# Optimization experiments

Hardware: AMD Instinct MI355X
Metric: run time of the kernel (lower is better)

## Reference

```python
import jax, jax.numpy as jnp
import numpy as np

D_MODEL = 1024
NUM_HEADS = 16
D_K = D_MODEL // NUM_HEADS
B, S = 4, 4096


def setup_inputs() -> dict:
    key = jax.random.key(0)
    ks = jax.random.split(key, 12)
    sc = 1.0 / np.sqrt(D_MODEL)
    inp = {
        "query": jax.random.normal(ks[0], (B, S, D_MODEL), dtype=jnp.float32),
        "key": jax.random.normal(ks[1], (B, S, D_MODEL), dtype=jnp.float32),
        "value": jax.random.normal(ks[2], (B, S, D_MODEL), dtype=jnp.float32),
        "w_q": jax.random.normal(ks[3], (D_MODEL, D_MODEL), dtype=jnp.float32) * sc,
        "b_q": jax.random.normal(ks[4], (D_MODEL,), dtype=jnp.float32) * sc,
        "w_k": jax.random.normal(ks[5], (D_MODEL, D_MODEL), dtype=jnp.float32) * sc,
        "b_k": jax.random.normal(ks[6], (D_MODEL,), dtype=jnp.float32) * sc,
        "w_v": jax.random.normal(ks[7], (D_MODEL, D_MODEL), dtype=jnp.float32) * sc,
        "b_v": jax.random.normal(ks[8], (D_MODEL,), dtype=jnp.float32) * sc,
        "w_o": jax.random.normal(ks[9], (D_MODEL, D_MODEL), dtype=jnp.float32) * sc,
        "b_o": jax.random.normal(ks[10], (D_MODEL,), dtype=jnp.float32) * sc,
    }
    return inp


def reference(query, key, value, w_q, b_q, w_k, b_k, w_v, b_v, w_o, b_o):
    b, s, _ = query.shape
    # projections (torch Linear: x @ W.T + b)
    Q = query @ w_q.T + b_q
    K = key @ w_k.T + b_k
    V = value @ w_v.T + b_v
    # elu+1 feature map
    Q = jax.nn.elu(Q) + 1.0
    K = jax.nn.elu(K) + 1.0
    # [b, h, s, d]
    Q = Q.reshape(b, s, NUM_HEADS, D_K).transpose(0, 2, 1, 3)
    K = K.reshape(b, s, NUM_HEADS, D_K).transpose(0, 2, 1, 3)
    V = V.reshape(b, s, NUM_HEADS, D_K).transpose(0, 2, 1, 3)
    # KV outer-sum: [b, h, d, d]
    KV = jnp.einsum("bhsd,bhse->bhde", K, V)
    Z = jnp.einsum("bhsd,bhde->bhse", Q, KV)  # [b, h, s, d]
    Ksum = K.sum(axis=-2)  # [b, h, d]
    D = jnp.einsum("bhsd,bhd->bhs", Q, Ksum)[..., None]  # [b, h, s, 1]
    Z = Z / (D + 1e-6)
    Z = Z.transpose(0, 2, 1, 3).reshape(b, s, D_MODEL)
    return Z @ w_o.T + b_o
```

## Files before the change

### kernel.cpp

```cpp
#include <hip/hip_runtime.h>
#include <stdint.h>

#define DM 1024
#define NH 16
#define DKH 64
#define BB 4
#define SS 4096
#define MM (BB*SS)

typedef __bf16 bf16x8 __attribute__((ext_vector_type(8)));
typedef float f32x4 __attribute__((ext_vector_type(4)));

__device__ __forceinline__ float bf2f(ushort u) {
  union { uint32_t i; float f; } v; v.i = ((uint32_t)u) << 16; return v.f;
}
__device__ __forceinline__ ushort f2bf(float f) {
  union { float f; uint32_t i; } v; v.f = f;
  uint32_t x = v.i;
  uint32_t r = (x + 0x7fffu + ((x >> 16) & 1u)) >> 16;
  return (ushort)r;
}
__device__ __forceinline__ void unpack8(uint4 u, float* o) {
  o[0] = bf2f((ushort)(u.x & 0xffff)); o[1] = bf2f((ushort)(u.x >> 16));
  o[2] = bf2f((ushort)(u.y & 0xffff)); o[3] = bf2f((ushort)(u.y >> 16));
  o[4] = bf2f((ushort)(u.z & 0xffff)); o[5] = bf2f((ushort)(u.z >> 16));
  o[6] = bf2f((ushort)(u.w & 0xffff)); o[7] = bf2f((ushort)(u.w >> 16));
}
__device__ __forceinline__ void unpack4(uint2 u, float* o) {
  o[0] = bf2f((ushort)(u.x & 0xffff)); o[1] = bf2f((ushort)(u.x >> 16));
  o[2] = bf2f((ushort)(u.y & 0xffff)); o[3] = bf2f((ushort)(u.y >> 16));
}

#define GLL16(g, l) __builtin_amdgcn_global_load_lds( \
    (__attribute__((address_space(1))) void*)(g), \
    (__attribute__((address_space(3))) void*)(l), 16, 0, 0)

__global__ void cast_w4(const float* __restrict__ s0, const float* __restrict__ s1,
                        const float* __restrict__ s2, const float* __restrict__ s3,
                        ushort* __restrict__ d0, ushort* __restrict__ d1,
                        ushort* __restrict__ d2, ushort* __restrict__ d3) {
  const int which = blockIdx.x >> 10;
  const int i = ((blockIdx.x & 1023) * 256 + threadIdx.x) * 4;
  const float* src = which == 0 ? s0 : (which == 1 ? s1 : (which == 2 ? s2 : s3));
  ushort* dst = which == 0 ? d0 : (which == 1 ? d1 : (which == 2 ? d2 : d3));
  float4 v = *reinterpret_cast<const float4*>(src + i);
  ushort4 o; o.x = f2bf(v.x); o.y = f2bf(v.y); o.z = f2bf(v.z); o.w = f2bf(v.w);
  *reinterpret_cast<ushort4*>(dst + i) = o;
}

template<int MODE>
__global__ __launch_bounds__(512, 2) void gemm8p(
    const ushort* __restrict__ A, const ushort* __restrict__ Bw,
    const float* __restrict__ bias, void* __restrict__ Cout) {
  constexpr int K = DM, N = DM;
  constexpr int NT = K / 32;
  __shared__ ushort smem[4][2][256 * 32];
  const int t = threadIdx.x;
  const int lane = t & 63;
  const int w = t >> 6;
  const int id = blockIdx.y * gridDim.x + blockIdx.x;
  const int cpx = (gridDim.x * gridDim.y) >> 3;
  const int swz = (id & 7) * cpx + (id >> 3);
  const int bx = swz % gridDim.x;
  const int by = swz / gridDim.x;
  const int m0 = by * 256, n0 = bx * 256;
  const int wm = w >> 2, wn = w & 3;
  const int fr = lane & 15;
  const int slot = lane >> 4;

  const int gsw = ((t & 3) ^ ((t >> 2) & 3)) * 8;
  const size_t baseA = (size_t)(m0 + (t >> 2)) * K + gsw;
  const size_t baseB = (size_t)(n0 + (t >> 2)) * K + gsw;
  const int ldsoff = w * 512;

  f32x4 acc[8][4] = {};

#define STAGE(tile) { \
    const int _b = (tile) & 3; const size_t _k = (size_t)(tile) * 32; \
    GLL16(A + baseA + _k, &smem[_b][0][ldsoff]); \
    GLL16(A + baseA + (size_t)128 * K + _k, &smem[_b][0][4096 + ldsoff]); \
    GLL16(Bw + baseB + _k, &smem[_b][1][ldsoff]); \
    GLL16(Bw + baseB + (size_t)128 * K + _k, &smem[_b][1][4096 + ldsoff]); }

  STAGE(0); STAGE(1); STAGE(2);
  asm volatile("s_waitcnt vmcnt(8)" ::: "memory");
  __builtin_amdgcn_s_barrier();
  __builtin_amdgcn_sched_barrier(0);

  for (int p = 0; p < NT; ++p) {
    const ushort* At = &smem[p & 3][0][0];
    const ushort* Bt = &smem[p & 3][1][0];
    bf16x8 bfr[4], afr[8];
#pragma unroll
    for (int ni = 0; ni < 4; ++ni) {
      const int row = wn * 64 + ni * 16 + fr;
      bfr[ni] = *reinterpret_cast<const bf16x8*>(Bt + row * 32 + ((slot ^ (fr & 3)) << 3));
    }
#pragma unroll
    for (int mi = 0; mi < 8; ++mi) {
      const int row = wm * 128 + mi * 16 + fr;
      afr[mi] = *reinterpret_cast<const bf16x8*>(At + row * 32 + ((slot ^ (fr & 3)) << 3));
    }
    if (p + 3 < NT) STAGE(p + 3);
    __builtin_amdgcn_s_setprio(1);
#pragma unroll
    for (int mi = 0; mi < 8; ++mi)
#pragma unroll
      for (int ni = 0; ni < 4; ++ni)
        acc[mi][ni] = __builtin_amdgcn_mfma_f32_16x16x32_bf16(afr[mi], bfr[ni], acc[mi][ni], 0, 0, 0);
    __builtin_amdgcn_s_setprio(0);
    if (p < NT - 1) {
      if (p < NT - 3)       asm volatile("s_waitcnt vmcnt(8)" ::: "memory");
      else if (p == NT - 3) asm volatile("s_waitcnt vmcnt(4)" ::: "memory");
      else                  asm volatile("s_waitcnt vmcnt(0)" ::: "memory");
      __builtin_amdgcn_s_barrier();
      __builtin_amdgcn_sched_barrier(0);
    }
  }
#undef STAGE

  const int fq = (lane >> 4) * 4;
  float bv[4];
#pragma unroll
  for (int ni = 0; ni < 4; ++ni) bv[ni] = bias[n0 + wn * 64 + ni * 16 + fr];
#pragma unroll
  for (int mi = 0; mi < 8; ++mi) {
#pragma unroll
    for (int ni = 0; ni < 4; ++ni) {
      const int c = n0 + wn * 64 + ni * 16 + fr;
#pragma unroll
      for (int q = 0; q < 4; ++q) {
        const int r = m0 + wm * 128 + mi * 16 + fq + q;
        float v = acc[mi][ni][q] + bv[ni];
        if constexpr (MODE == 0) v = (v > 0.f) ? (v + 1.f) : __expf(v);
        if constexpr (MODE == 2) {
          reinterpret_cast<float*>(Cout)[(size_t)r * N + c] = v;
        } else {
          reinterpret_cast<ushort*>(Cout)[(size_t)r * N + c] = f2bf(v);
        }
      }
    }
  }
}

__global__ __launch_bounds__(512, 2) void gemm8pa(
    const float* __restrict__ Q32, const float* __restrict__ K32,
    const float* __restrict__ V32,
    const ushort* __restrict__ Wq, const ushort* __restrict__ Wk,
    const ushort* __restrict__ Wv,
    const float* __restrict__ bq, const float* __restrict__ bk,
    const float* __restrict__ bv_,
    ushort* __restrict__ Qp, ushort* __restrict__ Kp, ushort* __restrict__ Vp) {
  constexpr int K = DM, N = DM;
  constexpr int NT = K / 32;
  __shared__ float  smemA[3][256 * 32];
  __shared__ ushort smemB[3][256 * 32];
  const int bz = blockIdx.z;
  const float*  A32  = bz == 0 ? Q32 : (bz == 1 ? K32 : V32);
  const ushort* Bw   = bz == 0 ? Wq  : (bz == 1 ? Wk  : Wv);
  const float*  bias = bz == 0 ? bq  : (bz == 1 ? bk  : bv_);
  ushort*       Cout = bz == 0 ? Qp  : (bz == 1 ? Kp  : Vp);
  const bool do_elu = (bz != 2);

  const int t = threadIdx.x;
  const int lane = t & 63;
  const int w = t >> 6;
  const int id = blockIdx.y * gridDim.x + blockIdx.x;
  const int cpx = (gridDim.x * gridDim.y) >> 3;
  const int swz = (id & 7) * cpx + (id >> 3);
  const int bx = swz % gridDim.x;
  const int by = swz / gridDim.x;
  const int m0 = by * 256, n0 = bx * 256;
  const int wm = w >> 1, wn = w & 1;
  const int fr = lane & 15;
  const int slot = lane >> 4;

  const int gcolA = (((t & 7) ^ ((t >> 3) & 7)) << 2);
  const size_t baseAf = (size_t)(m0 + (t >> 3)) * K + gcolA;
  const int gsw = ((t & 3) ^ ((t >> 2) & 3)) * 8;
  const size_t baseB = (size_t)(n0 + (t >> 2)) * K + gsw;
  const int ldsoffB = w * 512;

  const int rx = lane & 7;
  const int sA0 = (((2 * slot) ^ rx) << 2);
  const int sA1 = (((2 * slot + 1) ^ rx) << 2);
  const int sB = ((slot ^ (fr & 3)) << 3);

  f32x4 acc[4][8] = {};

#define STAGEA(tile) { \
    const int _b = (tile) % 3; const size_t _k = (size_t)(tile) * 32; \
    GLL16(A32 + baseAf + _k,                      &smemA[_b][w * 256]); \
    GLL16(A32 + baseAf + (size_t) 64 * K + _k,    &smemA[_b][2048 + w * 256]); \
    GLL16(A32 + baseAf + (size_t)128 * K + _k,    &smemA[_b][4096 + w * 256]); \
    GLL16(A32 + baseAf + (size_t)192 * K + _k,    &smemA[_b][6144 + w * 256]); }
#define STAGEB(tile) { \
    const int _b = (tile) % 3; const size_t _k = (size_t)(tile) * 32; \
    GLL16(Bw + baseB + _k,                  &smemB[_b][ldsoffB]); \
    GLL16(Bw + baseB + (size_t)128 * K + _k, &smemB[_b][4096 + ldsoffB]); }

  STAGEA(0); STAGEB(0); STAGEA(1); STAGEB(1);
  asm volatile("s_waitcnt vmcnt(6)" ::: "memory");
  __builtin_amdgcn_s_barrier();
  __builtin_amdgcn_sched_barrier(0);

  for (int p = 0; p < NT; ++p) {
    const float*  At = &smemA[p % 3][0];
    const ushort* Bt = &smemB[p % 3][0];
    bf16x8 bfr[8], afr[4];
#pragma unroll
    for (int ni = 0; ni < 8; ++ni) {
      const int row = wn * 128 + ni * 16 + fr;
      bfr[ni] = *reinterpret_cast<const bf16x8*>(Bt + row * 32 + sB);
    }
#pragma unroll
    for (int mi = 0; mi < 4; ++mi) {
      const float* rbase = At + (wm * 64 + mi * 16 + fr) * 32;
      f32x4 a0 = *reinterpret_cast<const f32x4*>(rbase + sA0);
      f32x4 a1 = *reinterpret_cast<const f32x4*>(rbase + sA1);
      uint4 uu;
      asm("v_cvt_pk_bf16_f32 %0, %1, %2" : "=v"(uu.x) : "v"(a0[0]), "v"(a0[1]));
      asm("v_cvt_pk_bf16_f32 %0, %1, %2" : "=v"(uu.y) : "v"(a0[2]), "v"(a0[3]));
      asm("v_cvt_pk_bf16_f32 %0, %1, %2" : "=v"(uu.z) : "v"(a1[0]), "v"(a1[1]));
      asm("v_cvt_pk_bf16_f32 %0, %1, %2" : "=v"(uu.w) : "v"(a1[2]), "v"(a1[3]));
      afr[mi] = *reinterpret_cast<bf16x8*>(&uu);
    }
    if (p + 2 < NT) { STAGEA(p + 2); STAGEB(p + 2); }
    __builtin_amdgcn_s_setprio(1);
#pragma unroll
    for (int mi = 0; mi < 4; ++mi)
#pragma unroll
      for (int ni = 0; ni < 8; ++ni)
        acc[mi][ni] = __builtin_amdgcn_mfma_f32_16x16x32_bf16(afr[mi], bfr[ni], acc[mi][ni], 0, 0, 0);
    __builtin_amdgcn_s_setprio(0);
    if (p < NT - 1) {
      if (p < NT - 2) asm volatile("s_waitcnt vmcnt(6)" ::: "memory");
      else            asm volatile("s_waitcnt vmcnt(0)" ::: "memory");
      __builtin_amdgcn_s_barrier();
      __builtin_amdgcn_sched_barrier(0);
    }
  }
#undef STAGEA
#undef STAGEB

  const int fq = (lane >> 4) * 4;
  float bvv[8];
#pragma unroll
  for (int ni = 0; ni < 8; ++ni) bvv[ni] = bias[n0 + wn * 128 + ni * 16 + fr];
#pragma unroll
  for (int mi = 0; mi < 4; ++mi) {
#pragma unroll
    for (int ni = 0; ni < 8; ++ni) {
      const int c = n0 + wn * 128 + ni * 16 + fr;
#pragma unroll
      for (int q = 0; q < 4; ++q) {
        const int r = m0 + wm * 64 + mi * 16 + fq + q;
        float v = acc[mi][ni][q] + bvv[ni];
        if (do_elu) v = (v > 0.f) ? (v + 1.f) : __expf(v);
        Cout[(size_t)r * N + c] = f2bf(v);
      }
    }
  }
}

__global__ __launch_bounds__(256) void kv_kernel(
    const ushort* __restrict__ Kp, const ushort* __restrict__ Vp,
    float* __restrict__ KVpart, float* __restrict__ Kspart) {
  __shared__ ushort KL[4][64][64];
  __shared__ ushort VL[4][64][64];
  const int bh = blockIdx.x;
  const int chunk = blockIdx.y;
  const int b = bh >> 4, h = bh & 15;
  const int t = threadIdx.x;
  const int w = t >> 6, lane = t & 63;
  const int d0 = (lane >> 2) * 4;
  const int e0 = (lane & 3) * 16;
  const int srow = lane >> 3;
  const int scol = (lane & 7) * 8;

  float acc[4][16] = {};
  float ks[4] = {};

  ushort* lk = &KL[w][0][0];
  ushort* lv = &VL[w][0][0];
  const int s_wave = chunk * 512 + w * 128;

  for (int tile = 0; tile < 2; ++tile) {
    const int s0 = s_wave + tile * 64;
    const size_t gbase = (size_t)(b * SS + s0 + srow) * DM + h * 64 + scol;
    asm volatile("s_waitcnt lgkmcnt(0)" ::: "memory");
#pragma unroll
    for (int it = 0; it < 8; ++it) {
      GLL16(Kp + gbase + (size_t)it * 8 * DM, lk + it * 512);
      GLL16(Vp + gbase + (size_t)it * 8 * DM, lv + it * 512);
    }
    asm volatile("s_waitcnt vmcnt(0)" ::: "memory");
    __builtin_amdgcn_sched_barrier(0);

#pragma unroll 2
    for (int s = 0; s < 64; ++s) {
      float kf[4], vf[16];
      uint2 uk = *reinterpret_cast<const uint2*>(&KL[w][s][d0]);
      uint4 uv0 = *reinterpret_cast<const uint4*>(&VL[w][s][e0]);
      uint4 uv1 = *reinterpret_cast<const uint4*>(&VL[w][s][e0 + 8]);
      unpack4(uk, kf);
      unpack8(uv0, vf);
      unpack8(uv1, vf + 8);
#pragma unroll
      for (int i = 0; i < 4; ++i) {
        ks[i] += kf[i];
#pragma unroll
        for (int j = 0; j < 16; ++j) acc[i][j] += kf[i] * vf[j];
      }
    }
  }

  const int slab = chunk * 4 + w;
  float* kvp = KVpart + ((size_t)slab * 64 + bh) * 4096;
#pragma unroll
  for (int i = 0; i < 4; ++i) {
#pragma unroll
    for (int j4 = 0; j4 < 4; ++j4) {
      float4 v = { acc[i][j4*4+0], acc[i][j4*4+1], acc[i][j4*4+2], acc[i][j4*4+3] };
      *reinterpret_cast<float4*>(kvp + (d0 + i) * 64 + e0 + j4 * 4) = v;
    }
  }
  if ((lane & 3) == 0) {
    float4 v = { ks[0], ks[1], ks[2], ks[3] };
    *reinterpret_cast<float4*>(Kspart + (size_t)slab * 4096 + bh * 64 + d0) = v;
  }
}

__global__ __launch_bounds__(256) void kvreduce_kernel(
    const float* __restrict__ KVpart, const float* __restrict__ Kspart,
    ushort* __restrict__ KVTx) {
  const int idx = blockIdx.x * 256 + threadIdx.x;
  const int bh = idx >> 12;
  const int d = (idx >> 6) & 63;
  const int e = idx & 63;
  float s = 0.f;
#pragma unroll
  for (int c = 0; c < 32; ++c) s += KVpart[(size_t)c * (64 * 4096) + idx];
  KVTx[(size_t)bh * 5120 + e * 64 + d] = f2bf(s);
  if (idx < 64 * 64) {
    float s2 = 0.f;
#pragma unroll
    for (int c = 0; c < 32; ++c) s2 += Kspart[(size_t)c * 4096 + idx];
    KVTx[(size_t)(idx >> 6) * 5120 + 4096 + (idx & 63)] = f2bf(s2);
  }
}

__global__ __launch_bounds__(256) void z_mfma_kernel(
    const ushort* __restrict__ Qp, const ushort* __restrict__ KVTx,
    ushort* __restrict__ Zn) {
  const int bh = blockIdx.y;
  const int b = bh >> 4, h = bh & 15;
  const int t = threadIdx.x;
  const int w = t >> 6, lane = t & 63;
  const int fr = lane & 15;
  const int kq = (lane >> 4) * 8;
  const int s0 = blockIdx.x * 128 + w * 32;

  const ushort* kvb = KVTx + (size_t)bh * 5120;
  bf16x8 bfrag[5][2];
#pragma unroll
  for (int ni = 0; ni < 5; ++ni)
#pragma unroll
    for (int ks = 0; ks < 2; ++ks)
      bfrag[ni][ks] = *reinterpret_cast<const bf16x8*>(kvb + (ni * 16 + fr) * 64 + ks * 32 + kq);

  f32x4 acc[2][5] = {};
  const size_t arow = (size_t)(b * SS + s0 + fr) * DM + h * 64;
#pragma unroll
  for (int mi = 0; mi < 2; ++mi) {
#pragma unroll
    for (int ks = 0; ks < 2; ++ks) {
      bf16x8 a = *reinterpret_cast<const bf16x8*>(Qp + arow + (size_t)mi * 16 * DM + ks * 32 + kq);
#pragma unroll
      for (int ni = 0; ni < 5; ++ni)
        acc[mi][ni] = __builtin_amdgcn_mfma_f32_16x16x32_bf16(a, bfrag[ni][ks], acc[mi][ni], 0, 0, 0);
    }
  }

#pragma unroll
  for (int mi = 0; mi < 2; ++mi) {
#pragma unroll
    for (int q = 0; q < 4; ++q) {
      const float dv = __shfl(acc[mi][4][q], lane & 48);
      const float inv = 1.f / (dv + 1e-6f);
      const int r = s0 + mi * 16 + (lane >> 4) * 4 + q;
      ushort* orow = Zn + (size_t)(b * SS + r) * DM + h * 64;
#pragma unroll
      for (int ni = 0; ni < 4; ++ni)
        orow[ni * 16 + fr] = f2bf(acc[mi][ni][q] * inv);
    }
  }
}

extern "C" void kernel_launch(void* const* d_in, const int* in_sizes, int n_in,
                              void* d_out, int out_size, void* d_ws, size_t ws_size,
                              hipStream_t stream) {
  const float* query = (const float*)d_in[0];
  const float* key_  = (const float*)d_in[1];
  const float* value = (const float*)d_in[2];
  const float* w_q = (const float*)d_in[3];
  const float* b_q = (const float*)d_in[4];
  const float* w_k = (const float*)d_in[5];
  const float* b_k = (const float*)d_in[6];
  const float* w_v = (const float*)d_in[7];
  const float* b_v = (const float*)d_in[8];
  const float* w_o = (const float*)d_in[9];
  const float* b_o = (const float*)d_in[10];

  char* ws = (char*)d_ws;
  const size_t NX = (size_t)MM * DM;
  ushort* Wq = (ushort*)ws; ws += (size_t)DM * DM * 2;
  ushort* Wk = (ushort*)ws; ws += (size_t)DM * DM * 2;
  ushort* Wv = (ushort*)ws; ws += (size_t)DM * DM * 2;
  ushort* Wo = (ushort*)ws; ws += (size_t)DM * DM * 2;
  ushort* Qp = (ushort*)ws; ws += NX * 2;
  ushort* Kp = (ushort*)ws; ws += NX * 2;
  ushort* Vp = (ushort*)ws; ws += NX * 2;
  float*  KVpart = (float*)ws; ws += (size_t)32 * 64 * 4096 * 4;
  float*  Kspart = (float*)ws; ws += (size_t)32 * 4096 * 4;
  ushort* KVTx = (ushort*)ws; ws += (size_t)64 * 80 * 64 * 2;
  ushort* Zn = (ushort*)ws; ws += NX * 2;

  cast_w4<<<4 * 1024, 256, 0, stream>>>(w_q, w_k, w_v, w_o, Wq, Wk, Wv, Wo);

  dim3 gg3(DM / 256, MM / 256, 3);
  gemm8pa<<<gg3, 512, 0, stream>>>(query, key_, value, Wq, Wk, Wv,
                                   b_q, b_k, b_v, Qp, Kp, Vp);

  kv_kernel<<<dim3(64, 8), 256, 0, stream>>>(Kp, Vp, KVpart, Kspart);
  hipMemsetAsync(KVTx, 0, (size_t)64 * 80 * 64 * 2, stream);
  kvreduce_kernel<<<1024, 256, 0, stream>>>(KVpart, Kspart, KVTx);
  z_mfma_kernel<<<dim3(32, 64), 256, 0, stream>>>(Qp, KVTx, Zn);

  dim3 gg(DM / 256, MM / 256);
  gemm8p<2><<<gg, 512, 0, stream>>>(Zn, Wo, b_o, d_out);
}
```

Before: 272.3 us.

## Load fp32 A operand directly into registers instead of staging through LDS

The QKV projection GEMM no longer copies the fp32 activation tiles into shared memory. Each wave now loads its own A rows straight into registers, one k-tile ahead, and converts them to bf16 there. Only the bf16 weight tiles stay triple-buffered in LDS, and the manual vmcnt waits are adjusted for the new load counts. This cuts LDS footprint and LDS read traffic, which may allow more resident blocks. In exchange, the two column-waves now each fetch the same A rows from global memory, 32 more VGPRs are used, and the prefetch is only one tile deep, so load latency can be exposed.

```diff
diff --git a/kernel.cpp b/kernel.cpp
--- a/kernel.cpp
+++ b/kernel.cpp
@@ -153,7 +153,6 @@
     ushort* __restrict__ Qp, ushort* __restrict__ Kp, ushort* __restrict__ Vp) {
   constexpr int K = DM, N = DM;
   constexpr int NT = K / 32;
-  __shared__ float  smemA[3][256 * 32];
   __shared__ ushort smemB[3][256 * 32];
   const int bz = blockIdx.z;
   const float*  A32  = bz == 0 ? Q32 : (bz == 1 ? K32 : V32);
@@ -175,37 +174,35 @@
   const int fr = lane & 15;
   const int slot = lane >> 4;
 
-  const int gcolA = (((t & 7) ^ ((t >> 3) & 7)) << 2);
-  const size_t baseAf = (size_t)(m0 + (t >> 3)) * K + gcolA;
   const int gsw = ((t & 3) ^ ((t >> 2) & 3)) * 8;
   const size_t baseB = (size_t)(n0 + (t >> 2)) * K + gsw;
   const int ldsoffB = w * 512;
-
-  const int rx = lane & 7;
-  const int sA0 = (((2 * slot) ^ rx) << 2);
-  const int sA1 = (((2 * slot + 1) ^ rx) << 2);
   const int sB = ((slot ^ (fr & 3)) << 3);
 
+  const size_t aBase = (size_t)(m0 + wm * 64 + fr) * K + slot * 8;
+
   f32x4 acc[4][8] = {};
-
-#define STAGEA(tile) { \
-    const int _b = (tile) % 3; const size_t _k = (size_t)(tile) * 32; \
-    GLL16(A32 + baseAf + _k,                      &smemA[_b][w * 256]); \
-    GLL16(A32 + baseAf + (size_t) 64 * K + _k,    &smemA[_b][2048 + w * 256]); \
-    GLL16(A32 + baseAf + (size_t)128 * K + _k,    &smemA[_b][4096 + w * 256]); \
-    GLL16(A32 + baseAf + (size_t)192 * K + _k,    &smemA[_b][6144 + w * 256]); }
+  uint4 S[8];
+
 #define STAGEB(tile) { \
     const int _b = (tile) % 3; const size_t _k = (size_t)(tile) * 32; \
-    GLL16(Bw + baseB + _k,                  &smemB[_b][ldsoffB]); \
+    GLL16(Bw + baseB + _k,                   &smemB[_b][ldsoffB]); \
     GLL16(Bw + baseB + (size_t)128 * K + _k, &smemB[_b][4096 + ldsoffB]); }
-
-  STAGEA(0); STAGEB(0); STAGEA(1); STAGEB(1);
-  asm volatile("s_waitcnt vmcnt(6)" ::: "memory");
+#define AISSUE(tile) { \
+    _Pragma("unroll") \
+    for (int mi = 0; mi < 4; ++mi) { \
+      const float* _p = A32 + aBase + (size_t)mi * 16 * K + (size_t)(tile) * 32; \
+      S[2 * mi]     = *reinterpret_cast<const uint4*>(_p); \
+      S[2 * mi + 1] = *reinterpret_cast<const uint4*>(_p + 4); \
+    } }
+
+  AISSUE(0);
+  STAGEB(0); STAGEB(1);
+  asm volatile("s_waitcnt vmcnt(2)" ::: "memory");
   __builtin_amdgcn_s_barrier();
   __builtin_amdgcn_sched_barrier(0);
 
   for (int p = 0; p < NT; ++p) {
-    const float*  At = &smemA[p % 3][0];
     const ushort* Bt = &smemB[p % 3][0];
     bf16x8 bfr[8], afr[4];
 #pragma unroll
@@ -215,17 +212,17 @@
     }
 #pragma unroll
     for (int mi = 0; mi < 4; ++mi) {
-      const float* rbase = At + (wm * 64 + mi * 16 + fr) * 32;
-      f32x4 a0 = *reinterpret_cast<const f32x4*>(rbase + sA0);
-      f32x4 a1 = *reinterpret_cast<const f32x4*>(rbase + sA1);
+      const float* f0 = reinterpret_cast<const float*>(&S[2 * mi]);
+      const float* f1 = reinterpret_cast<const float*>(&S[2 * mi + 1]);
       uint4 uu;
-      asm("v_cvt_pk_bf16_f32 %0, %1, %2" : "=v"(uu.x) : "v"(a0[0]), "v"(a0[1]));
-      asm("v_cvt_pk_bf16_f32 %0, %1, %2" : "=v"(uu.y) : "v"(a0[2]), "v"(a0[3]));
-      asm("v_cvt_pk_bf16_f32 %0, %1, %2" : "=v"(uu.z) : "v"(a1[0]), "v"(a1[1]));
-      asm("v_cvt_pk_bf16_f32 %0, %1, %2" : "=v"(uu.w) : "v"(a1[2]), "v"(a1[3]));
+      asm("v_cvt_pk_bf16_f32 %0, %1, %2" : "=v"(uu.x) : "v"(f0[0]), "v"(f0[1]));
+      asm("v_cvt_pk_bf16_f32 %0, %1, %2" : "=v"(uu.y) : "v"(f0[2]), "v"(f0[3]));
+      asm("v_cvt_pk_bf16_f32 %0, %1, %2" : "=v"(uu.z) : "v"(f1[0]), "v"(f1[1]));
+      asm("v_cvt_pk_bf16_f32 %0, %1, %2" : "=v"(uu.w) : "v"(f1[2]), "v"(f1[3]));
       afr[mi] = *reinterpret_cast<bf16x8*>(&uu);
     }
-    if (p + 2 < NT) { STAGEA(p + 2); STAGEB(p + 2); }
+    if (p + 1 < NT) AISSUE(p + 1);
+    if (p + 2 < NT) STAGEB(p + 2);
     __builtin_amdgcn_s_setprio(1);
 #pragma unroll
     for (int mi = 0; mi < 4; ++mi)
@@ -234,13 +231,13 @@
         acc[mi][ni] = __builtin_amdgcn_mfma_f32_16x16x32_bf16(afr[mi], bfr[ni], acc[mi][ni], 0, 0, 0);
     __builtin_amdgcn_s_setprio(0);
     if (p < NT - 1) {
-      if (p < NT - 2) asm volatile("s_waitcnt vmcnt(6)" ::: "memory");
-      else            asm volatile("s_waitcnt vmcnt(0)" ::: "memory");
+      if (p < NT - 2) asm volatile("s_waitcnt vmcnt(10)" ::: "memory");
+      else            asm volatile("s_waitcnt vmcnt(8)" ::: "memory");
       __builtin_amdgcn_s_barrier();
       __builtin_amdgcn_sched_barrier(0);
     }
   }
-#undef STAGEA
+#undef AISSUE
 #undef STAGEB
 
   const int fq = (lane >> 4) * 4;
```

Result: slower. 353.8 us (+30.0%).

## Load QKV-projection weights directly into registers and deepen fp32 activation pipeline

Applied to the files above, without the earlier changes.

The fused QKV projection GEMM no longer stages the bf16 weight tile through LDS. Each wave now loads its B fragments straight from global memory into double-buffered registers one tile ahead. The freed shared memory goes to a four-stage fp32 activation ring, prefetched three tiles ahead, with the vmcnt waits adjusted to match. This removes LDS traffic and bank pressure for B and adds load latency hiding. The cost is more VGPRs (16 uint4 buffers), which risks spills under the 512x2 launch bound, and uncoalesced, redundant global reads of the weights across waves.

```diff
diff --git a/kernel.cpp b/kernel.cpp
--- a/kernel.cpp
+++ b/kernel.cpp
@@ -143,7 +143,7 @@
   }
 }
 
-__global__ __launch_bounds__(512, 2) void gemm8pa(
+__global__ __launch_bounds__(512, 2) void gemm8pb(
     const float* __restrict__ Q32, const float* __restrict__ K32,
     const float* __restrict__ V32,
     const ushort* __restrict__ Wq, const ushort* __restrict__ Wk,
@@ -153,8 +153,7 @@
     ushort* __restrict__ Qp, ushort* __restrict__ Kp, ushort* __restrict__ Vp) {
   constexpr int K = DM, N = DM;
   constexpr int NT = K / 32;
-  __shared__ float  smemA[3][256 * 32];
-  __shared__ ushort smemB[3][256 * 32];
+  __shared__ float smemA[4][256 * 32];
   const int bz = blockIdx.z;
   const float*  A32  = bz == 0 ? Q32 : (bz == 1 ? K32 : V32);
   const ushort* Bw   = bz == 0 ? Wq  : (bz == 1 ? Wk  : Wv);
@@ -177,71 +176,71 @@
 
   const int gcolA = (((t & 7) ^ ((t >> 3) & 7)) << 2);
   const size_t baseAf = (size_t)(m0 + (t >> 3)) * K + gcolA;
-  const int gsw = ((t & 3) ^ ((t >> 2) & 3)) * 8;
-  const size_t baseB = (size_t)(n0 + (t >> 2)) * K + gsw;
-  const int ldsoffB = w * 512;
-
   const int rx = lane & 7;
   const int sA0 = (((2 * slot) ^ rx) << 2);
   const int sA1 = (((2 * slot + 1) ^ rx) << 2);
-  const int sB = ((slot ^ (fr & 3)) << 3);
+  const size_t bBase = (size_t)(n0 + wn * 128 + fr) * K + slot * 8;
 
   f32x4 acc[4][8] = {};
+  uint4 RB0[8], RB1[8];
 
 #define STAGEA(tile) { \
-    const int _b = (tile) % 3; const size_t _k = (size_t)(tile) * 32; \
-    GLL16(A32 + baseAf + _k,                      &smemA[_b][w * 256]); \
-    GLL16(A32 + baseAf + (size_t) 64 * K + _k,    &smemA[_b][2048 + w * 256]); \
-    GLL16(A32 + baseAf + (size_t)128 * K + _k,    &smemA[_b][4096 + w * 256]); \
-    GLL16(A32 + baseAf + (size_t)192 * K + _k,    &smemA[_b][6144 + w * 256]); }
-#define STAGEB(tile) { \
-    const int _b = (tile) % 3; const size_t _k = (size_t)(tile) * 32; \
-    GLL16(Bw + baseB + _k,                  &smemB[_b][ldsoffB]); \
-    GLL16(Bw + baseB + (size_t)128 * K + _k, &smemB[_b][4096 + ldsoffB]); }
-
-  STAGEA(0); STAGEB(0); STAGEA(1); STAGEB(1);
-  asm volatile("s_waitcnt vmcnt(6)" ::: "memory");
+    const int _b = (tile) & 3; const size_t _k = (size_t)(tile) * 32; \
+    GLL16(A32 + baseAf + _k,                   &smemA[_b][w * 256]); \
+    GLL16(A32 + baseAf + (size_t) 64 * K + _k, &smemA[_b][2048 + w * 256]); \
+    GLL16(A32 + baseAf + (size_t)128 * K + _k, &smemA[_b][4096 + w * 256]); \
+    GLL16(A32 + baseAf + (size_t)192 * K + _k, &smemA[_b][6144 + w * 256]); }
+#define BLOAD(tile, RS) { \
+    _Pragma("unroll") \
+    for (int ni = 0; ni < 8; ++ni) \
+      RS[ni] = *reinterpret_cast<const uint4*>(Bw + bBase + (size_t)ni * 16 * K + (size_t)(tile) * 32); }
+
+  STAGEA(0); STAGEA(1); STAGEA(2);
+  BLOAD(0, RB0);
+  asm volatile("s_waitcnt vmcnt(16)" ::: "memory");
   __builtin_amdgcn_s_barrier();
   __builtin_amdgcn_sched_barrier(0);
 
-  for (int p = 0; p < NT; ++p) {
-    const float*  At = &smemA[p % 3][0];
-    const ushort* Bt = &smemB[p % 3][0];
-    bf16x8 bfr[8], afr[4];
-#pragma unroll
-    for (int ni = 0; ni < 8; ++ni) {
-      const int row = wn * 128 + ni * 16 + fr;
-      bfr[ni] = *reinterpret_cast<const bf16x8*>(Bt + row * 32 + sB);
-    }
-#pragma unroll
-    for (int mi = 0; mi < 4; ++mi) {
-      const float* rbase = At + (wm * 64 + mi * 16 + fr) * 32;
-      f32x4 a0 = *reinterpret_cast<const f32x4*>(rbase + sA0);
-      f32x4 a1 = *reinterpret_cast<const f32x4*>(rbase + sA1);
-      uint4 uu;
-      asm("v_cvt_pk_bf16_f32 %0, %1, %2" : "=v"(uu.x) : "v"(a0[0]), "v"(a0[1]));
-      asm("v_cvt_pk_bf16_f32 %0, %1, %2" : "=v"(uu.y) : "v"(a0[2]), "v"(a0[3]));
-      asm("v_cvt_pk_bf16_f32 %0, %1, %2" : "=v"(uu.z) : "v"(a1[0]), "v"(a1[1]));
-      asm("v_cvt_pk_bf16_f32 %0, %1, %2" : "=v"(uu.w) : "v"(a1[2]), "v"(a1[3]));
-      afr[mi] = *reinterpret_cast<bf16x8*>(&uu);
-    }
-    if (p + 2 < NT) { STAGEA(p + 2); STAGEB(p + 2); }
-    __builtin_amdgcn_s_setprio(1);
-#pragma unroll
-    for (int mi = 0; mi < 4; ++mi)
-#pragma unroll
-      for (int ni = 0; ni < 8; ++ni)
-        acc[mi][ni] = __builtin_amdgcn_mfma_f32_16x16x32_bf16(afr[mi], bfr[ni], acc[mi][ni], 0, 0, 0);
-    __builtin_amdgcn_s_setprio(0);
-    if (p < NT - 1) {
-      if (p < NT - 2) asm volatile("s_waitcnt vmcnt(6)" ::: "memory");
-      else            asm volatile("s_waitcnt vmcnt(0)" ::: "memory");
-      __builtin_amdgcn_s_barrier();
-      __builtin_amdgcn_sched_barrier(0);
-    }
-  }
+#define PHASE(p, CS, IS) { \
+    const float* At = &smemA[(p) & 3][0]; \
+    bf16x8 afr[4]; \
+    _Pragma("unroll") \
+    for (int mi = 0; mi < 4; ++mi) { \
+      const float* rbase = At + (wm * 64 + mi * 16 + fr) * 32; \
+      f32x4 a0 = *reinterpret_cast<const f32x4*>(rbase + sA0); \
+      f32x4 a1 = *reinterpret_cast<const f32x4*>(rbase + sA1); \
+      uint4 uu; \
+      asm("v_cvt_pk_bf16_f32 %0, %1, %2" : "=v"(uu.x) : "v"(a0[0]), "v"(a0[1])); \
+      asm("v_cvt_pk_bf16_f32 %0, %1, %2" : "=v"(uu.y) : "v"(a0[2]), "v"(a0[3])); \
+      asm("v_cvt_pk_bf16_f32 %0, %1, %2" : "=v"(uu.z) : "v"(a1[0]), "v"(a1[1])); \
+      asm("v_cvt_pk_bf16_f32 %0, %1, %2" : "=v"(uu.w) : "v"(a1[2]), "v"(a1[3])); \
+      afr[mi] = *reinterpret_cast<bf16x8*>(&uu); \
+    } \
+    if ((p) + 1 < NT) BLOAD((p) + 1, IS); \
+    if ((p) + 3 < NT) STAGEA((p) + 3); \
+    __builtin_amdgcn_s_setprio(1); \
+    _Pragma("unroll") \
+    for (int mi = 0; mi < 4; ++mi) \
+      _Pragma("unroll") \
+      for (int ni = 0; ni < 8; ++ni) \
+        acc[mi][ni] = __builtin_amdgcn_mfma_f32_16x16x32_bf16( \
+            afr[mi], *reinterpret_cast<const bf16x8*>(&CS[ni]), acc[mi][ni], 0, 0, 0); \
+    __builtin_amdgcn_s_setprio(0); \
+    if ((p) < NT - 1) { \
+      if ((p) <= NT - 4)      asm volatile("s_waitcnt vmcnt(24)" ::: "memory"); \
+      else if ((p) == NT - 3) asm volatile("s_waitcnt vmcnt(20)" ::: "memory"); \
+      else                    asm volatile("s_waitcnt vmcnt(16)" ::: "memory"); \
+      __builtin_amdgcn_s_barrier(); \
+      __builtin_amdgcn_sched_barrier(0); \
+    } }
+
+  for (int pp = 0; pp < NT; pp += 2) {
+    PHASE(pp, RB0, RB1);
+    PHASE(pp + 1, RB1, RB0);
+  }
+#undef PHASE
+#undef BLOAD
 #undef STAGEA
-#undef STAGEB
 
   const int fq = (lane >> 4) * 4;
   float bvv[8];
@@ -429,11 +428,11 @@
   cast_w4<<<4 * 1024, 256, 0, stream>>>(w_q, w_k, w_v, w_o, Wq, Wk, Wv, Wo);
 
   dim3 gg3(DM / 256, MM / 256, 3);
-  gemm8pa<<<gg3, 512, 0, stream>>>(query, key_, value, Wq, Wk, Wv,
+  gemm8pb<<<gg3, 512, 0, stream>>>(query, key_, value, Wq, Wk, Wv,
                                    b_q, b_k, b_v, Qp, Kp, Vp);
 
   kv_kernel<<<dim3(64, 8), 256, 0, stream>>>(Kp, Vp, KVpart, Kspart);
-  hipMemsetAsync(KVTx, 0, (size_t)64 * 80 * 64 * 2, stream);
+  (void)hipMemsetAsync(KVTx, 0, (size_t)64 * 80 * 64 * 2, stream);
   kvreduce_kernel<<<1024, 256, 0, stream>>>(KVpart, Kspart, KVTx);
   z_mfma_kernel<<<dim3(32, 64), 256, 0, stream>>>(Qp, KVTx, Zn);
 
```

Result: slower. 395.3 us (+45.2%).
